# Kernel optimization log

Measured on AMD Instinct MI355X. Metric: run time of the kernel, lower is better.

## Reference

```python
import math
import jax, jax.numpy as jnp
import numpy as np

D_MODEL = 768
N_HEADS = 12


def setup_inputs() -> dict:
    key = jax.random.key(0)
    kx, kw, kb = jax.random.split(key, 3)
    x = jax.random.normal(kx, (2, 2048, D_MODEL), dtype=jnp.float32)
    # nn.Linear(D, 3D): weight [3D, D], bias [3D]; init ~ U(-1/sqrt(D), 1/sqrt(D))
    bound = 1.0 / math.sqrt(D_MODEL)
    W_kqv = jax.random.uniform(kw, (3 * D_MODEL, D_MODEL), dtype=jnp.float32, minval=-bound, maxval=bound)
    b_kqv = jax.random.uniform(kb, (3 * D_MODEL,), dtype=jnp.float32, minval=-bound, maxval=bound)
    return {"x": x, "W_kqv": W_kqv, "b_kqv": b_kqv}


def reference(x, W_kqv, b_kqv):
    N, C, D = x.shape
    H = N_HEADS
    hd = D // H
    z = jnp.einsum('ncd,ed->nce', x, W_kqv) + b_kqv  # [N, C, 3D]
    # order in source: k first, then q, then v
    k = z[:, :, :D].reshape(N, C, H, hd).transpose(0, 2, 1, 3)       # [N,H,C,hd]
    q = z[:, :, D:2 * D].reshape(N, C, H, hd).transpose(0, 2, 1, 3)
    v = z[:, :, 2 * D:].reshape(N, C, H, hd).transpose(0, 2, 1, 3)
    # NOTE: faithful to source: scale by sqrt(D) (full model dim), not sqrt(head_dim)
    scores = jnp.einsum('nhqd,nhkd->nhqk', q, k) / math.sqrt(D)
    causal = jnp.tril(jnp.ones((C, C), dtype=bool))
    scores = jnp.where(causal, scores, -jnp.inf)
    attn = jax.nn.softmax(scores, axis=-1)
    out = jnp.einsum('nhqk,nhkd->nhqd', attn, v)  # [N,H,C,hd]
    return out.transpose(0, 2, 1, 3).reshape(N, C, D)
```

## Files before the change

### kernel.cpp

```cpp
#include <hip/hip_runtime.h>
#include <stdint.h>

#define D_MODEL 768
#define E3      2304
#define NCTX    2048
#define NH      12
#define HD      64
#define MROWS   4096
#define NHTOT   24

typedef __attribute__((ext_vector_type(8))) short short8;
typedef __attribute__((ext_vector_type(4))) short bf16x4;
typedef __attribute__((ext_vector_type(4))) float f32x4;

typedef __attribute__((address_space(3))) uint32_t lds_u32;
typedef __attribute__((address_space(1))) uint32_t glob_u32;

__device__ __forceinline__ void async_copy16(const void* g, void* l) {
    __builtin_amdgcn_global_load_lds((const glob_u32*)(uintptr_t)g,
                                     (lds_u32*)(uint32_t)(uintptr_t)l, 16, 0, 0);
}

__device__ __forceinline__ unsigned short f2bf(float f) {
    uint32_t u = __builtin_bit_cast(uint32_t, f);
    u += 0x7fffu + ((u >> 16) & 1u);
    return (unsigned short)(u >> 16);
}

__device__ __forceinline__ float fast_exp2(float x) {
#if __has_builtin(__builtin_amdgcn_exp2f)
    return __builtin_amdgcn_exp2f(x);
#else
    return __expf(x * 0.6931471805599453f);
#endif
}

__device__ __forceinline__ f32x4 mfma16_bf16(bf16x4 a, bf16x4 b, f32x4 c) {
#if defined(__HIP_DEVICE_COMPILE__)
    return __builtin_amdgcn_mfma_f32_16x16x16bf16_1k(a, b, c, 0, 0, 0);
#else
    (void)a; (void)b;
    return c;
#endif
}

__global__ void cast_bf16_kernel(const float* __restrict__ in, unsigned short* __restrict__ out) {
    int i = blockIdx.x * blockDim.x + threadIdx.x;
    float4 v = ((const float4*)in)[i];
    ushort4 o;
    o.x = f2bf(v.x); o.y = f2bf(v.y); o.z = f2bf(v.z); o.w = f2bf(v.w);
    ((ushort4*)out)[i] = o;
}

__global__ __launch_bounds__(256) void qkv_gemm(const unsigned short* __restrict__ A,
                                                const unsigned short* __restrict__ B,
                                                const float* __restrict__ bias,
                                                unsigned short* __restrict__ Zq,
                                                unsigned short* __restrict__ Kb,
                                                unsigned short* __restrict__ Vb) {
    __shared__ __attribute__((aligned(16))) unsigned short sA[128 * 64];
    __shared__ __attribute__((aligned(16))) unsigned short sB[96 * 64];

    const int tid  = threadIdx.x;
    const int wave = tid >> 6;
    const int lane = tid & 63;
    const int quad = lane >> 4;
    const int l15  = lane & 15;
    const int wm   = (wave >> 1) * 64;
    const int wn   = (wave & 1) * 48;

    const int id   = blockIdx.x;
    const int by   = (id & 7) * 4 + ((id >> 3) & 3);
    const int bx   = id >> 5;
    const int row0 = by * 128;
    const int col0 = bx * 96;

    const int srow   = lane & 7;
    const int schunk = (lane >> 3) * 8;

    f32x4 acc[4][3] = {};

    for (int k0 = 0; k0 < D_MODEL; k0 += 64) {
        __syncthreads();
#pragma unroll
        for (int c = 0; c < 4; ++c) {
            const int reg = wave * 4 + c;
            async_copy16(A + (size_t)(row0 + reg * 8 + srow) * D_MODEL + k0 + schunk, &sA[reg * 512]);
        }
#pragma unroll
        for (int c = 0; c < 3; ++c) {
            const int reg = wave * 3 + c;
            async_copy16(B + (size_t)(col0 + reg * 8 + srow) * D_MODEL + k0 + schunk, &sB[reg * 512]);
        }
        __syncthreads();

#pragma unroll
        for (int ks = 0; ks < 2; ++ks) {
            const int qoff = (ks * 4 + quad) * 64 + (l15 & 7) * 8;
            short8 aF[4], bF[3];
#pragma unroll
            for (int i = 0; i < 4; ++i)
                aF[i] = *(const short8*)&sA[((wm >> 3) + i * 2 + (l15 >> 3)) * 512 + qoff];
#pragma unroll
            for (int j = 0; j < 3; ++j)
                bF[j] = *(const short8*)&sB[((wn >> 3) + j * 2 + (l15 >> 3)) * 512 + qoff];
#pragma unroll
            for (int i = 0; i < 4; ++i)
#pragma unroll
                for (int j = 0; j < 3; ++j)
                    acc[i][j] = __builtin_amdgcn_mfma_f32_16x16x32_bf16(aF[i], bF[j], acc[i][j], 0, 0, 0);
        }
    }

    if (col0 < D_MODEL) {
#pragma unroll
        for (int j = 0; j < 3; ++j) {
            const int col = col0 + wn + j * 16 + l15;
            const float bv = bias[col];
            const int h = col >> 6, d = col & 63;
            const int ks = d >> 5, quadd = (d >> 3) & 3, e = d & 7;
#pragma unroll
            for (int i = 0; i < 4; ++i) {
                const int row = row0 + wm + i * 16 + quad * 4;
                const int n = row >> 11;
                const int key = row & (NCTX - 1);
                const int kb = key >> 6;
                const int ct = (key >> 4) & 3;
                const size_t base = ((size_t)((n * NH + h) * 32 + kb)) * 4096
                                  + (((ks * 4 + ct) * 4 + quadd) * 16) * 8 + e;
#pragma unroll
                for (int r = 0; r < 4; ++r)
                    Kb[base + (size_t)(quad * 4 + r) * 8] = f2bf(acc[i][j][r] + bv);
            }
        }
    } else if (col0 < 2 * D_MODEL) {
        const float zscale = 0.036084391824351615f * 1.4426950408889634f;
#pragma unroll
        for (int j = 0; j < 3; ++j) {
            const int colz = col0 + wn + j * 16 + l15;
            const float bv = bias[colz];
            const int col = colz - D_MODEL;
#pragma unroll
            for (int i = 0; i < 4; ++i) {
                const int row = row0 + wm + i * 16 + quad * 4;
#pragma unroll
                for (int r = 0; r < 4; ++r)
                    Zq[(size_t)(row + r) * D_MODEL + col] = f2bf((acc[i][j][r] + bv) * zscale);
            }
        }
    } else {
#pragma unroll
        for (int j = 0; j < 3; ++j) {
            const int col = col0 + wn + j * 16 + l15;
            const float bv = bias[col];
            const int ch = col - 2 * D_MODEL;
            const int h = ch >> 6, d = ch & 63;
            const int dt = d >> 4, l15d = d & 15;
#pragma unroll
            for (int i = 0; i < 4; ++i) {
                const int row = row0 + wm + i * 16 + quad * 4;
                const int n = row >> 11;
                const int key = row & (NCTX - 1);
                const int kb = key >> 6;
                const int ct = (key >> 4) & 3;
                ushort4 w4;
                w4.x = f2bf(acc[i][j][0] + bv);
                w4.y = f2bf(acc[i][j][1] + bv);
                w4.z = f2bf(acc[i][j][2] + bv);
                w4.w = f2bf(acc[i][j][3] + bv);
                *(ushort4*)&Vb[((size_t)((n * NH + h) * 32 + kb)) * 4096
                               + (((ct * 4 + dt) * 4 + quad) * 16 + l15d) * 4] = w4;
            }
        }
    }
}

__global__ __launch_bounds__(256) void attn_kernel(const unsigned short* __restrict__ Zq,
                                                   const unsigned short* __restrict__ Kb,
                                                   const unsigned short* __restrict__ Vb,
                                                   float* __restrict__ out) {
    __shared__ __attribute__((aligned(16))) unsigned short sK[2][4096];
    __shared__ __attribute__((aligned(16))) unsigned short sV[2][4096];

    const int tid  = threadIdx.x;
    const int wave = tid >> 6;
    const int lane = tid & 63;
    const int quad = lane >> 4;
    const int l15  = lane & 15;
    const int b    = blockIdx.x;
    const int nh   = b % NHTOT;
    const int t    = (NCTX / 64 - 1) - b / NHTOT;
    const int n    = nh / NH;
    const int h    = nh - n * NH;

    const unsigned short* KbP = Kb + (size_t)(nh * 32) * 4096;
    const unsigned short* VbP = Vb + (size_t)(nh * 32) * 4096;

    const unsigned short* Qp = Zq + (size_t)(n * NCTX + t * 64 + wave * 16) * D_MODEL + h * HD;
    short8 qf[2];
#pragma unroll
    for (int ks = 0; ks < 2; ++ks)
        qf[ks] = *(const short8*)&Qp[(size_t)l15 * D_MODEL + ks * 32 + quad * 8];

    f32x4 o[4] = {};
    float lsum = 0.0f;

#pragma unroll
    for (int c = 0; c < 2; ++c) {
        const int off = wave * 1024 + c * 512;
        async_copy16(KbP + off + lane * 8, &sK[0][off]);
        async_copy16(VbP + off + lane * 8, &sV[0][off]);
    }

    for (int kb = 0; kb <= t; ++kb) {
        const int buf = kb & 1;
        __syncthreads();
        if (kb < t) {
#pragma unroll
            for (int c = 0; c < 2; ++c) {
                const int off = wave * 1024 + c * 512;
                async_copy16(KbP + (size_t)(kb + 1) * 4096 + off + lane * 8, &sK[buf ^ 1][off]);
                async_copy16(VbP + (size_t)(kb + 1) * 4096 + off + lane * 8, &sV[buf ^ 1][off]);
            }
        }

        short8 kf[2][4];
#pragma unroll
        for (int ks = 0; ks < 2; ++ks)
#pragma unroll
            for (int ct = 0; ct < 4; ++ct)
                kf[ks][ct] = *(const short8*)&sK[buf][(ks * 4 + ct) * 512 + lane * 8];

        f32x4 s[4] = {};
#pragma unroll
        for (int ct = 0; ct < 4; ++ct) {
            s[ct] = __builtin_amdgcn_mfma_f32_16x16x32_bf16(kf[0][ct], qf[0], s[ct], 0, 0, 0);
            s[ct] = __builtin_amdgcn_mfma_f32_16x16x32_bf16(kf[1][ct], qf[1], s[ct], 0, 0, 0);
        }

        const bool diag = (kb == t);
        const int qg = t * 64 + wave * 16 + l15;
        bf16x4 pA[4];
#pragma unroll
        for (int ct = 0; ct < 4; ++ct) {
            float pv[4];
#pragma unroll
            for (int r = 0; r < 4; ++r) {
                const int key = kb * 64 + ct * 16 + quad * 4 + r;
                float sv = s[ct][r];
                if (diag && key > qg) sv = -INFINITY;
                pv[r] = fast_exp2(sv);
                lsum += pv[r];
            }
            pA[ct][0] = (short)f2bf(pv[0]); pA[ct][1] = (short)f2bf(pv[1]);
            pA[ct][2] = (short)f2bf(pv[2]); pA[ct][3] = (short)f2bf(pv[3]);
        }

#pragma unroll
        for (int ct = 0; ct < 4; ++ct)
#pragma unroll
            for (int dt = 0; dt < 4; ++dt) {
                const bf16x4 vf = *(const bf16x4*)&sV[buf][(ct * 4 + dt) * 256 + lane * 4];
                o[dt] = mfma16_bf16(pA[ct], vf, o[dt]);
            }
    }

    float l = lsum;
    l += __shfl_xor(l, 16);
    l += __shfl_xor(l, 32);
    const float linv = 1.0f / l;
#pragma unroll
    for (int r = 0; r < 4; ++r) {
        const float inv = __shfl(linv, quad * 4 + r);
        const size_t row = (size_t)n * NCTX + t * 64 + wave * 16 + quad * 4 + r;
#pragma unroll
        for (int dt = 0; dt < 4; ++dt)
            out[row * D_MODEL + h * HD + dt * 16 + l15] = o[dt][r] * inv;
    }
}

extern "C" void kernel_launch(void* const* d_in, const int* in_sizes, int n_in,
                              void* d_out, int out_size, void* d_ws, size_t ws_size,
                              hipStream_t stream) {
    const float* x = (const float*)d_in[0];
    const float* W = (const float*)d_in[1];
    const float* b = (const float*)d_in[2];
    float* out = (float*)d_out;

    unsigned short* xb = (unsigned short*)d_ws;
    unsigned short* Wb = xb + (size_t)MROWS * D_MODEL;
    unsigned short* Zq = Wb + (size_t)E3 * D_MODEL;
    unsigned short* Kb = Zq + (size_t)MROWS * D_MODEL;
    unsigned short* Vb = Kb + (size_t)NHTOT * 32 * 4096;

    cast_bf16_kernel<<<dim3((MROWS * D_MODEL / 4) / 256), 256, 0, stream>>>(x, xb);
    cast_bf16_kernel<<<dim3((E3 * D_MODEL / 4) / 256), 256, 0, stream>>>(W, Wb);
    qkv_gemm<<<dim3(768), 256, 0, stream>>>(xb, Wb, b, Zq, Kb, Vb);
    attn_kernel<<<dim3(NHTOT * (NCTX / 64)), 256, 0, stream>>>(Zq, Kb, Vb, out);
}
```

Before: 146.5 us.

## Rewrite QKV GEMM to load fragments directly from global with register double-buffering

The QKV projection GEMM drops LDS staging and barriers. Each of two waves per block now computes a 64x96 tile, loading MFMA operand fragments straight from global memory into registers. Loads for the next k-slice are double-buffered against the current MFMAs. This removes LDS traffic and __syncthreads stalls, but it roughly doubles global/L2 reads because B fragments are no longer shared across waves, and it raises register pressure with fewer waves per block.

```diff
diff --git a/kernel.cpp b/kernel.cpp
--- a/kernel.cpp
+++ b/kernel.cpp
@@ -52,76 +52,59 @@
     ((ushort4*)out)[i] = o;
 }
 
-__global__ __launch_bounds__(256) void qkv_gemm(const unsigned short* __restrict__ A,
+__global__ __launch_bounds__(128) void qkv_gemm(const unsigned short* __restrict__ A,
                                                 const unsigned short* __restrict__ B,
                                                 const float* __restrict__ bias,
                                                 unsigned short* __restrict__ Zq,
                                                 unsigned short* __restrict__ Kb,
                                                 unsigned short* __restrict__ Vb) {
-    __shared__ __attribute__((aligned(16))) unsigned short sA[128 * 64];
-    __shared__ __attribute__((aligned(16))) unsigned short sB[96 * 64];
-
     const int tid  = threadIdx.x;
     const int wave = tid >> 6;
     const int lane = tid & 63;
     const int quad = lane >> 4;
     const int l15  = lane & 15;
-    const int wm   = (wave >> 1) * 64;
-    const int wn   = (wave & 1) * 48;
-
-    const int id   = blockIdx.x;
-    const int by   = (id & 7) * 4 + ((id >> 3) & 3);
-    const int bx   = id >> 5;
-    const int row0 = by * 128;
-    const int col0 = bx * 96;
-
-    const int srow   = lane & 7;
-    const int schunk = (lane >> 3) * 8;
-
-    f32x4 acc[4][3] = {};
-
+
+    const int id = blockIdx.x;
+    const int by = (id & 7) * 4 + ((id >> 3) & 3);
+    const int bx = id >> 5;
+    const int row0  = by * 128 + wave * 64;
+    const int col0  = bx * 96;
+
+    const unsigned short* Abase = A + (size_t)(row0 + l15) * D_MODEL + quad * 8;
+    const unsigned short* Bbase = B + (size_t)(col0 + l15) * D_MODEL + quad * 8;
+
+    short8 a0[4], b0[6], a1[4], b1[6];
+#define LOAD_A(dst, k)  _Pragma("unroll") for (int i = 0; i < 4; ++i) \
+    dst[i] = *(const short8*)(Abase + (size_t)i * 16 * D_MODEL + (k));
+#define LOAD_B(dst, k)  _Pragma("unroll") for (int j = 0; j < 6; ++j) \
+    dst[j] = *(const short8*)(Bbase + (size_t)j * 16 * D_MODEL + (k));
+#define MFMA_ALL(af, bf) _Pragma("unroll") for (int i = 0; i < 4; ++i) \
+    _Pragma("unroll") for (int j = 0; j < 6; ++j) \
+        acc[i][j] = __builtin_amdgcn_mfma_f32_16x16x32_bf16(af[i], bf[j], acc[i][j], 0, 0, 0);
+
+    f32x4 acc[4][6] = {};
+
+    LOAD_A(a0, 0) LOAD_B(b0, 0)
     for (int k0 = 0; k0 < D_MODEL; k0 += 64) {
-        __syncthreads();
-#pragma unroll
-        for (int c = 0; c < 4; ++c) {
-            const int reg = wave * 4 + c;
-            async_copy16(A + (size_t)(row0 + reg * 8 + srow) * D_MODEL + k0 + schunk, &sA[reg * 512]);
-        }
-#pragma unroll
-        for (int c = 0; c < 3; ++c) {
-            const int reg = wave * 3 + c;
-            async_copy16(B + (size_t)(col0 + reg * 8 + srow) * D_MODEL + k0 + schunk, &sB[reg * 512]);
-        }
-        __syncthreads();
-
-#pragma unroll
-        for (int ks = 0; ks < 2; ++ks) {
-            const int qoff = (ks * 4 + quad) * 64 + (l15 & 7) * 8;
-            short8 aF[4], bF[3];
-#pragma unroll
-            for (int i = 0; i < 4; ++i)
-                aF[i] = *(const short8*)&sA[((wm >> 3) + i * 2 + (l15 >> 3)) * 512 + qoff];
-#pragma unroll
-            for (int j = 0; j < 3; ++j)
-                bF[j] = *(const short8*)&sB[((wn >> 3) + j * 2 + (l15 >> 3)) * 512 + qoff];
-#pragma unroll
-            for (int i = 0; i < 4; ++i)
-#pragma unroll
-                for (int j = 0; j < 3; ++j)
-                    acc[i][j] = __builtin_amdgcn_mfma_f32_16x16x32_bf16(aF[i], bF[j], acc[i][j], 0, 0, 0);
-        }
-    }
+        if (k0 + 32 < D_MODEL) { LOAD_A(a1, k0 + 32) LOAD_B(b1, k0 + 32) }
+        MFMA_ALL(a0, b0)
+        if (k0 + 64 < D_MODEL) { LOAD_A(a0, k0 + 64) LOAD_B(b0, k0 + 64) }
+        MFMA_ALL(a1, b1)
+    }
+#undef LOAD_A
+#undef LOAD_B
+#undef MFMA_ALL
 
     if (col0 < D_MODEL) {
 #pragma unroll
-        for (int j = 0; j < 3; ++j) {
-            const int col = col0 + wn + j * 16 + l15;
+        for (int j = 0; j < 6; ++j) {
+            const int col = col0 + j * 16 + l15;
             const float bv = bias[col];
             const int h = col >> 6, d = col & 63;
             const int ks = d >> 5, quadd = (d >> 3) & 3, e = d & 7;
 #pragma unroll
             for (int i = 0; i < 4; ++i) {
-                const int row = row0 + wm + i * 16 + quad * 4;
+                const int row = row0 + i * 16 + quad * 4;
                 const int n = row >> 11;
                 const int key = row & (NCTX - 1);
                 const int kb = key >> 6;
@@ -136,13 +119,13 @@
     } else if (col0 < 2 * D_MODEL) {
         const float zscale = 0.036084391824351615f * 1.4426950408889634f;
 #pragma unroll
-        for (int j = 0; j < 3; ++j) {
-            const int colz = col0 + wn + j * 16 + l15;
+        for (int j = 0; j < 6; ++j) {
+            const int colz = col0 + j * 16 + l15;
             const float bv = bias[colz];
             const int col = colz - D_MODEL;
 #pragma unroll
             for (int i = 0; i < 4; ++i) {
-                const int row = row0 + wm + i * 16 + quad * 4;
+                const int row = row0 + i * 16 + quad * 4;
 #pragma unroll
                 for (int r = 0; r < 4; ++r)
                     Zq[(size_t)(row + r) * D_MODEL + col] = f2bf((acc[i][j][r] + bv) * zscale);
@@ -150,15 +133,15 @@
         }
     } else {
 #pragma unroll
-        for (int j = 0; j < 3; ++j) {
-            const int col = col0 + wn + j * 16 + l15;
+        for (int j = 0; j < 6; ++j) {
+            const int col = col0 + j * 16 + l15;
             const float bv = bias[col];
             const int ch = col - 2 * D_MODEL;
             const int h = ch >> 6, d = ch & 63;
             const int dt = d >> 4, l15d = d & 15;
 #pragma unroll
             for (int i = 0; i < 4; ++i) {
-                const int row = row0 + wm + i * 16 + quad * 4;
+                const int row = row0 + i * 16 + quad * 4;
                 const int n = row >> 11;
                 const int key = row & (NCTX - 1);
                 const int kb = key >> 6;
@@ -295,6 +278,6 @@
 
     cast_bf16_kernel<<<dim3((MROWS * D_MODEL / 4) / 256), 256, 0, stream>>>(x, xb);
     cast_bf16_kernel<<<dim3((E3 * D_MODEL / 4) / 256), 256, 0, stream>>>(W, Wb);
-    qkv_gemm<<<dim3(768), 256, 0, stream>>>(xb, Wb, b, Zq, Kb, Vb);
+    qkv_gemm<<<dim3(768), 128, 0, stream>>>(xb, Wb, b, Zq, Kb, Vb);
     attn_kernel<<<dim3(NHTOT * (NCTX / 64)), 256, 0, stream>>>(Zq, Kb, Vb, out);
 }
```

Result: slower. 164.9 us (+12.6%).
